# Kernel optimization log

Measured on AMD Instinct MI355X. Metric: run time of the kernel, lower is better.

Reference implementation:

```python
import jax, jax.numpy as jnp
import numpy as np
import math


def setup_inputs() -> dict:
    key = jax.random.key(0)
    ks = jax.random.split(key, 10)
    B, N, C, heads = 16, 1024, 256, 8
    nW = 4
    ANGLE_BINS = 5
    inner = C  # dim_head*heads == dim
    return {
        "x": jax.random.normal(ks[0], (B, N, C), jnp.float32),
        "mask": jax.random.normal(ks[1], (nW, N, N), jnp.float32),
        "affine_matrix": jax.random.normal(ks[2], (B, 2, 3), jnp.float32),
        "Wq": jax.random.normal(ks[3], (C, inner), jnp.float32) * (C ** -0.5),
        "bq": jnp.zeros((inner,), jnp.float32),
        "Wkv": jax.random.normal(ks[4], (C, 2 * inner), jnp.float32) * (C ** -0.5),
        "bkv": jnp.zeros((2 * inner,), jnp.float32),
        "Wp": jax.random.normal(ks[5], (C, C), jnp.float32) * (C ** -0.5),
        "bp": jnp.zeros((C,), jnp.float32),
        "angle_table": jnp.ones((ANGLE_BINS, heads), jnp.float32),
        "H": 32,
        "W": 32,
    }


def reference(x, mask, affine_matrix, Wq, bq, Wkv, bkv, Wp, bp, angle_table, H, W):
    B, N, C = x.shape
    heads = angle_table.shape[1]
    hd = C // heads
    scale = hd ** -0.5

    # qkv projections (torch Linear -> x @ W + b with W stored as (in, out))
    q = (x @ Wq + bq).reshape(B, N, heads, hd).transpose(0, 2, 1, 3)      # (B,h,N,d)
    kv = (x @ Wkv + bkv).reshape(B, N, 2, heads, hd).transpose(2, 0, 3, 1, 4)
    k, v = kv[0], kv[1]                                                    # (B,h,N,d)

    attn = jnp.einsum('bhqd,bhkd->bhqk', q * scale, k)                     # (B,h,N,N)

    # angle bias: per-query multiplicative bias in (1,2)
    grid_y, grid_x = jnp.meshgrid(jnp.arange(H), jnp.arange(W), indexing='ij')
    coords = jnp.stack([grid_x.reshape(-1), grid_y.reshape(-1)], -1).astype(jnp.float32)  # (N,2)
    center = jnp.array([W / 2.0, H / 2.0], jnp.float32)
    ego = jnp.einsum('bij,j->bi', affine_matrix[:, :2, :2], center) + affine_matrix[:, :2, 2]  # (B,2)
    rel = coords[None, :, :] - ego[:, None, :]                             # (B,N,2)
    ang = jnp.arctan2(rel[..., 1], rel[..., 0])
    bins = (((ang + math.pi) / (2.0 * math.pi)) * (angle_table.shape[0] - 1)).astype(jnp.int32)
    bias = 1.0 + jax.nn.sigmoid(angle_table[bins])                         # (B,N,h)
    attn = attn * bias.transpose(0, 2, 1)[..., None]                       # broadcast over keys

    # additive window mask then softmax
    nW = mask.shape[0]
    attn = attn.reshape(B // nW, nW, heads, N, N) + mask[None, :, None]
    attn = jax.nn.softmax(attn.reshape(B, heads, N, N), axis=-1)

    out = jnp.einsum('bhqk,bhkd->bhqd', attn, v).transpose(0, 2, 1, 3).reshape(B, N, C)
    return out @ Wp + bp
```

## Files before the change

kernel.cpp:

```cpp
#include <hip/hip_runtime.h>
#include <hip/hip_bf16.h>
#include <math.h>

#define BB 16
#define NTOK 1024
#define CDIM 256
#define HEADS 8
#define HD 32
#define LOG2E 1.4426950408889634f
#define PSHIFT 18.0f

typedef __attribute__((ext_vector_type(8))) _Float16 half8;
typedef __attribute__((ext_vector_type(8))) unsigned short u16x8;
typedef __attribute__((ext_vector_type(4))) unsigned int u32x4;
typedef __attribute__((ext_vector_type(4))) float f32x4;

__device__ __forceinline__ unsigned short f2h(float f) {
  _Float16 h = (_Float16)f;
  return __builtin_bit_cast(unsigned short, h);
}
__device__ __forceinline__ half8 ldh8(const unsigned short* p) {
  return *reinterpret_cast<const half8*>(p);
}
__device__ __forceinline__ void gl_lds16(const void* g, void* l) {
  __builtin_amdgcn_global_load_lds(
      (const __attribute__((address_space(1))) unsigned int*)g,
      (__attribute__((address_space(3))) unsigned int*)l, 16, 0, 0);
}

__global__ __launch_bounds__(256) void prep_xwb(
    const float* __restrict__ X, const float* __restrict__ Wq,
    const float* __restrict__ Wkv, const float* __restrict__ Wp,
    const float* __restrict__ affine, const float* __restrict__ atab,
    unsigned short* __restrict__ x16, unsigned short* __restrict__ wt16,
    unsigned short* __restrict__ wp16, float* __restrict__ bias) {
  int bid = blockIdx.x;
  if (bid < 2048) {
    size_t base = ((size_t)bid * 256 + threadIdx.x) * 8;
    float4 a = *(const float4*)(X + base);
    float4 b = *(const float4*)(X + base + 4);
    u16x8 o = {f2h(a.x), f2h(a.y), f2h(a.z), f2h(a.w),
               f2h(b.x), f2h(b.y), f2h(b.z), f2h(b.w)};
    *(u16x8*)(x16 + base) = o;
  } else if (bid < 3072) {
    int idx = (bid - 2048) * 256 + threadIdx.x;
    float val; size_t dst; bool isp = false;
    if (idx < 65536) {
      int k = idx >> 8, n = idx & 255;
      val = Wq[idx]; dst = (size_t)n * 256 + k;
    } else if (idx < 196608) {
      int i2 = idx - 65536;
      int k = i2 >> 9, n2 = i2 & 511;
      val = Wkv[i2]; dst = (size_t)(256 + n2) * 256 + k;
    } else {
      int i3 = idx - 196608;
      int k = i3 >> 8, n = i3 & 255;
      val = Wp[i3]; dst = (size_t)n * 256 + k; isp = true;
    }
    unsigned short h = f2h(val);
    if (isp) wp16[dst] = h; else wt16[dst] = h;
  } else {
    int idx = (bid - 3072) * 256 + threadIdx.x;
    if (idx >= BB * NTOK) return;
    int b = idx >> 10, n = idx & (NTOK - 1);
    float cx = (float)(n & 31);
    float cy = (float)(n >> 5);
    const float* A = affine + b * 6;
    float egx = fmaf(A[0], 16.f, fmaf(A[1], 16.f, A[2]));
    float egy = fmaf(A[3], 16.f, fmaf(A[4], 16.f, A[5]));
    float ang = atan2f(cy - egy, cx - egx);
    float t = (ang + 3.14159265358979323846f) *
              (1.f / (2.f * 3.14159265358979323846f)) * 4.f;
    int bin = (int)t;
    bin = bin < 0 ? 0 : (bin > 4 ? 4 : bin);
    for (int h = 0; h < HEADS; ++h) {
      float a = atab[bin * HEADS + h];
      float s = 1.f / (1.f + __expf(-a));
      bias[((size_t)b * HEADS + h) * NTOK + n] = 1.f + s;
    }
  }
}

__global__ __launch_bounds__(512, 4) void gemm_qkv16(
    const unsigned short* __restrict__ x16, const unsigned short* __restrict__ wt16,
    const float* __restrict__ bq, const float* __restrict__ bkv,
    const float* __restrict__ bias, const float* __restrict__ mask,
    unsigned short* __restrict__ q16, unsigned short* __restrict__ k16,
    unsigned short* __restrict__ vt16, float* __restrict__ mF32) {
  __shared__ __align__(16) unsigned short SM[16384];
  int bid = blockIdx.x;
  if (bid >= 768) {
    int idx = (bid - 768) * 512 + threadIdx.x;
    int b4 = idx >> 18;
    int rem = idx & 262143;
    int q = rem >> 8;
    int k = (rem & 255) * 4;
    float4 v = *(const float4*)(mask + ((size_t)b4 * NTOK + q) * NTOK + k);
    int kt = k >> 5;
    size_t off = (size_t)q * 16 + ((k & 31) >> 1);
    size_t slabE = ((size_t)(b4 * 64 + kt * 2)) * 16384;
    float2 e = {fmaf(v.x, LOG2E, -PSHIFT), fmaf(v.z, LOG2E, -PSHIFT)};
    float2 o = {fmaf(v.y, LOG2E, -PSHIFT), fmaf(v.w, LOG2E, -PSHIFT)};
    *(float2*)(mF32 + slabE + off) = e;
    *(float2*)(mF32 + slabE + 16384 + off) = o;
    return;
  }
  unsigned short* Xs = SM;
  unsigned short* Ws = SM + 8192;
  int tid = threadIdx.x;
  int w = tid >> 6, l = tid & 63;
  int row16 = l & 15, grp = l >> 4;
  int xcd = bid & 7, local = bid >> 3;
  int jb = local % 6, mb = xcd * 16 + local / 6;
  int j0 = jb * 128, m0 = mb * 128;
  int wm = w >> 1, wn = w & 1;

  auto stg = [&](int nb, int kt) {
    int k0s = kt * 32;
    int row = w * 16 + (l >> 2);
    int ge = (((l & 3) * 16) ^ ((row & 3) << 4)) >> 1;
    gl_lds16(x16 + (size_t)(m0 + row) * 256 + k0s + ge, Xs + nb * 4096 + w * 512);
    gl_lds16(wt16 + (size_t)(j0 + row) * 256 + k0s + ge, Ws + nb * 4096 + w * 512);
  };
  auto off16 = [&](int row, int g) {
    return row * 32 + ((((g * 16) ^ ((row & 3) << 4))) >> 1);
  };

  stg(0, 0);
  __syncthreads();

  f32x4 acc[2][4];
#pragma unroll
  for (int i = 0; i < 2; ++i)
#pragma unroll
    for (int c = 0; c < 4; ++c) acc[i][c] = (f32x4){0.f, 0.f, 0.f, 0.f};

  for (int kt = 0; kt < 8; ++kt) {
    int cur = kt & 1;
    if (kt < 7) stg(cur ^ 1, kt + 1);
    half8 a0 = ldh8(Xs + cur * 4096 + off16(wm * 32 + row16, grp));
    half8 a1 = ldh8(Xs + cur * 4096 + off16(wm * 32 + 16 + row16, grp));
#pragma unroll
    for (int c = 0; c < 4; ++c) {
      half8 bh = ldh8(Ws + cur * 4096 + off16(wn * 64 + c * 16 + row16, grp));
      acc[0][c] = __builtin_amdgcn_mfma_f32_16x16x32_f16(a0, bh, acc[0][c], 0, 0, 0);
      acc[1][c] = __builtin_amdgcn_mfma_f32_16x16x32_f16(a1, bh, acc[1][c], 0, 0, 0);
    }
    __syncthreads();
  }

  const float scaleq = 0.17677669529663687f * LOG2E;
  int half_mine = wm >> 1;
  for (int half = 0; half < 2; ++half) {
    if (half_mine == half) {
#pragma unroll
      for (int i = 0; i < 2; ++i) {
#pragma unroll
        for (int c = 0; c < 4; ++c) {
          int col = wn * 64 + c * 16 + row16;
          int jg = j0 + col;
#pragma unroll
          for (int r = 0; r < 4; ++r) {
            int rowl = (wm & 1) * 32 + i * 16 + grp * 4 + r;
            int m = m0 + half * 64 + rowl;
            int b = m >> 10, n = m & (NTOK - 1);
            float val = acc[i][c][r];
            unsigned short o;
            if (jb < 2)
              o = f2h((val + bq[jg]) * scaleq *
                      bias[((size_t)b * HEADS + (jg >> 5)) * NTOK + n]);
            else
              o = f2h(val + bkv[jg - CDIM]);
            SM[rowl * 136 + col] = o;
          }
        }
      }
    }
    __syncthreads();
    if (jb < 4) {
#pragma unroll
      for (int it = 0; it < 2; ++it) {
        int lin = it * 512 + tid;
        int rowb = lin >> 4, oct = lin & 15;
        u16x8 v = *(const u16x8*)&SM[rowb * 136 + oct * 8];
        int m = m0 + half * 64 + rowb;
        int b = m >> 10, n = m & (NTOK - 1);
        int jg = j0 + oct * 8;
        unsigned short* dst; int h, d;
        if (jb < 2) { h = jg >> 5; d = jg & 31; dst = q16; }
        else { int c2 = jg - CDIM; h = c2 >> 5; d = c2 & 31; dst = k16; }
        *(u16x8*)(dst + (((size_t)b * HEADS + h) * NTOK + n) * HD + d) = v;
      }
    } else {
#pragma unroll
      for (int it = 0; it < 2; ++it) {
        int lin = it * 512 + tid;
        int noct = lin >> 7, jl = lin & 127;
        u16x8 v;
#pragma unroll
        for (int e = 0; e < 8; ++e) v[e] = SM[(noct * 8 + e) * 136 + jl];
        int c3 = j0 + jl - 2 * CDIM;
        int h = c3 >> 5, d = c3 & 31;
        int n0 = m0 + half * 64 + noct * 8;
        int b = n0 >> 10, nn = n0 & (NTOK - 1);
        *(u16x8*)(vt16 + (((size_t)b * HEADS + h) * HD + d) * NTOK + nn) = v;
      }
    }
    __syncthreads();
  }
}

__global__ __launch_bounds__(512, 8) void attn16(
    const unsigned short* __restrict__ q16, const unsigned short* __restrict__ k16,
    const unsigned short* __restrict__ vt16, const float* __restrict__ mF32,
    unsigned short* __restrict__ ao16) {
  __shared__ __align__(16) unsigned short KT[2][2][1024];
  __shared__ __align__(16) unsigned short VT[2][2][1024];
  __shared__ __align__(16) float MT[2][2][1024];

  int tid = threadIdx.x;
  int w = tid >> 6, l = tid & 63;
  int row16 = l & 15, grp = l >> 4;
  int bid = blockIdx.x;
  int g = (bid >> 7) * 8 + (bid & 7);
  int inner = (bid >> 3) & 15;
  int qt = g >> 2, b4 = g & 3;
  int brep = inner >> 2, hg = inner & 3;
  int b = brep * 4 + b4;
  int hl = w & 1, role = w >> 1;
  int head = hg * 2 + hl;
  int bh = b * HEADS + head;
  int q0g = qt * 64;

  half8 bq16 = ldh8(q16 + ((size_t)bh * NTOK + q0g + role * 16 + row16) * HD +
                    grp * 8);

  const float* mFb = mF32 + (size_t)b4 * 64 * 16384;

  f32x4 acc[2];
  acc[0] = (f32x4){0.f, 0.f, 0.f, 0.f};
  acc[1] = (f32x4){0.f, 0.f, 0.f, 0.f};
  f32x4 accL = (f32x4){0.f, 0.f, 0.f, 0.f};
  const _Float16 one = (_Float16)1.0f;
  const half8 vones = {one, one, one, one, one, one, one, one};

  auto off32 = [&](int row, int gg) {
    return row * 32 + ((gg ^ ((row >> 1) & 3)) << 3);
  };

  auto stage = [&](int nb, int kt2) {
    int k0n = (kt2 & 31) * 32;
    if (role < 2) {
      int c = role;
      int r = c * 16 + (l >> 2);
      int key = 2 * (l >> 2) + c;
      int sk = (l & 3) ^ ((r >> 1) & 3);
      gl_lds16(k16 + ((size_t)bh * NTOK + k0n + key) * HD + sk * 8,
               &KT[nb][hl][c * 512]);
    } else {
      int c = role - 2;
      int dl = c * 16 + (l >> 2);
      int sv = (l & 3) ^ ((dl >> 1) & 3);
      gl_lds16(vt16 + ((size_t)bh * HD + dl) * NTOK + k0n + sv * 8,
               &VT[nb][hl][c * 512]);
    }
    {
      int slab = w >> 2, ch = w & 3;
      gl_lds16(mFb + (size_t)((kt2 & 31) * 2 + slab) * 16384 + q0g * 16 +
                   ch * 256 + l * 4,
               &MT[nb][slab][ch * 256]);
    }
  };

  stage(0, 0);
  __syncthreads();

  for (int kt = 0; kt < 32; ++kt) {
    int cur = kt & 1;
    if (kt < 31) stage(cur ^ 1, kt + 1);

    half8 kf0 = ldh8(&KT[cur][hl][off32(row16, grp)]);
    half8 kf1 = ldh8(&KT[cur][hl][off32(16 + row16, grp)]);
    half8 v0 = ldh8(&VT[cur][hl][off32(row16, grp)]);
    half8 v1 = ldh8(&VT[cur][hl][off32(16 + row16, grp)]);

    int qr = role * 16 + row16;
    f32x4 mC0 = *(const f32x4*)&MT[cur][0][qr * 16 + grp * 4];
    f32x4 mC1 = *(const f32x4*)&MT[cur][1][qr * 16 + grp * 4];
    f32x4 s0 = __builtin_amdgcn_mfma_f32_16x16x32_f16(kf0, bq16, mC0, 0, 0, 0);
    f32x4 s1 = __builtin_amdgcn_mfma_f32_16x16x32_f16(kf1, bq16, mC1, 0, 0, 0);
    f32x4 e0, e1;
#pragma unroll
    for (int r = 0; r < 4; ++r) {
      e0[r] = __builtin_amdgcn_exp2f(s0[r]);
      e1[r] = __builtin_amdgcn_exp2f(s1[r]);
    }
    u32x4 pk;
#pragma unroll
    for (int r = 0; r < 4; ++r)
      pk[r] = __builtin_bit_cast(unsigned,
                                 __builtin_amdgcn_cvt_pkrtz(e0[r], e1[r]));
    half8 pa = __builtin_bit_cast(half8, pk);
    acc[0] = __builtin_amdgcn_mfma_f32_16x16x32_f16(pa, v0, acc[0], 0, 0, 0);
    acc[1] = __builtin_amdgcn_mfma_f32_16x16x32_f16(pa, v1, acc[1], 0, 0, 0);
    accL = __builtin_amdgcn_mfma_f32_16x16x32_f16(pa, vones, accL, 0, 0, 0);
    __syncthreads();
  }

#pragma unroll
  for (int r = 0; r < 4; ++r) {
    float inv = 1.f / accL[r];
    int qrow = q0g + role * 16 + grp * 4 + r;
    size_t obase = ((size_t)b * NTOK + qrow) * CDIM + head * HD;
    ao16[obase + row16] = f2h(acc[0][r] * inv);
    ao16[obase + 16 + row16] = f2h(acc[1][r] * inv);
  }
}

__global__ __launch_bounds__(512, 4) void gemm_out16(
    const unsigned short* __restrict__ a16, const unsigned short* __restrict__ wp16,
    const float* __restrict__ bp, float* __restrict__ out) {
  __shared__ __align__(16) unsigned short SM[16384];
  unsigned short* Xs = SM;
  unsigned short* Ws = SM + 8192;
  int tid = threadIdx.x;
  int w = tid >> 6, l = tid & 63;
  int row16 = l & 15, grp = l >> 4;
  int bid = blockIdx.x;
  int xcd = bid & 7, local = bid >> 3;
  int jb = local & 1, mb = xcd * 16 + (local >> 1);
  int j0 = jb * 128, m0 = mb * 128;
  int wm = w >> 1, wn = w & 1;

  auto stg = [&](int nb, int kt) {
    int k0s = kt * 32;
    int row = w * 16 + (l >> 2);
    int ge = (((l & 3) * 16) ^ ((row & 3) << 4)) >> 1;
    gl_lds16(a16 + (size_t)(m0 + row) * 256 + k0s + ge, Xs + nb * 4096 + w * 512);
    gl_lds16(wp16 + (size_t)(j0 + row) * 256 + k0s + ge, Ws + nb * 4096 + w * 512);
  };
  auto off16 = [&](int row, int g) {
    return row * 32 + ((((g * 16) ^ ((row & 3) << 4))) >> 1);
  };

  stg(0, 0);
  __syncthreads();

  f32x4 acc[2][4];
#pragma unroll
  for (int i = 0; i < 2; ++i)
#pragma unroll
    for (int c = 0; c < 4; ++c) acc[i][c] = (f32x4){0.f, 0.f, 0.f, 0.f};

  for (int kt = 0; kt < 8; ++kt) {
    int cur = kt & 1;
    if (kt < 7) stg(cur ^ 1, kt + 1);
    half8 a0 = ldh8(Xs + cur * 4096 + off16(wm * 32 + row16, grp));
    half8 a1 = ldh8(Xs + cur * 4096 + off16(wm * 32 + 16 + row16, grp));
#pragma unroll
    for (int c = 0; c < 4; ++c) {
      half8 bh = ldh8(Ws + cur * 4096 + off16(wn * 64 + c * 16 + row16, grp));
      acc[0][c] = __builtin_amdgcn_mfma_f32_16x16x32_f16(a0, bh, acc[0][c], 0, 0, 0);
      acc[1][c] = __builtin_amdgcn_mfma_f32_16x16x32_f16(a1, bh, acc[1][c], 0, 0, 0);
    }
    __syncthreads();
  }

#pragma unroll
  for (int i = 0; i < 2; ++i) {
    int ng = m0 + wm * 32 + i * 16 + grp * 4;
#pragma unroll
    for (int c = 0; c < 4; ++c) {
      int jg = j0 + wn * 64 + c * 16 + row16;
      float bias = bp[jg];
#pragma unroll
      for (int r = 0; r < 4; ++r) {
        out[(size_t)(ng + r) * CDIM + jg] = acc[i][c][r] + bias;
      }
    }
  }
}

extern "C" void kernel_launch(void* const* d_in, const int* in_sizes, int n_in,
                              void* d_out, int out_size, void* d_ws,
                              size_t ws_size, hipStream_t stream) {
  const float* x = (const float*)d_in[0];
  const float* mask = (const float*)d_in[1];
  const float* affine = (const float*)d_in[2];
  const float* Wq = (const float*)d_in[3];
  const float* bq = (const float*)d_in[4];
  const float* Wkv = (const float*)d_in[5];
  const float* bkv = (const float*)d_in[6];
  const float* Wp = (const float*)d_in[7];
  const float* bp = (const float*)d_in[8];
  const float* atab = (const float*)d_in[9];
  float* out = (float*)d_out;

  const size_t bhnd = (size_t)BB * HEADS * NTOK * HD;
  unsigned short* q16 = (unsigned short*)d_ws;
  unsigned short* k16 = q16 + bhnd;
  unsigned short* vt16 = k16 + bhnd;
  unsigned short* x16 = vt16 + bhnd;
  unsigned short* wt16 = x16 + bhnd;
  unsigned short* wp16 = wt16 + 768 * 256;
  float* mF32 = (float*)(wp16 + 256 * 256);
  float* bias = mF32 + (size_t)4 * 64 * 16384;

  prep_xwb<<<3136, 256, 0, stream>>>(x, Wq, Wkv, Wp, affine, atab, x16, wt16,
                                     wp16, bias);
  gemm_qkv16<<<2816, 512, 0, stream>>>(x16, wt16, bq, bkv, bias, mask, q16,
                                       k16, vt16, mF32);
  attn16<<<1024, 512, 0, stream>>>(q16, k16, vt16, mF32, x16);
  gemm_out16<<<256, 512, 0, stream>>>(x16, wp16, bp, out);
}
```

Measured before the change: 82.50 us.

## Read raw mask directly in attention instead of pre-permuted copy

Removes the pre-pass that rewrote the 16 MB fp32 mask into a permuted, pre-scaled layout inside the QKV GEMM launch. The attention kernel now loads raw mask rows into LDS with an XOR swizzle, shuffles the values into the MFMA accumulator layout, and applies the log2e scale and shift to the scores before exp2. This saves one full write and read of the mask buffer. In exchange the inner loop gains an extra FMA per score, some register shuffling, and a changed scale on q, which alters numerics slightly.

```diff
diff --git a/kernel.cpp b/kernel.cpp
--- a/kernel.cpp
+++ b/kernel.cpp
@@ -84,27 +84,10 @@
 __global__ __launch_bounds__(512, 4) void gemm_qkv16(
     const unsigned short* __restrict__ x16, const unsigned short* __restrict__ wt16,
     const float* __restrict__ bq, const float* __restrict__ bkv,
-    const float* __restrict__ bias, const float* __restrict__ mask,
-    unsigned short* __restrict__ q16, unsigned short* __restrict__ k16,
-    unsigned short* __restrict__ vt16, float* __restrict__ mF32) {
+    const float* __restrict__ bias, unsigned short* __restrict__ q16,
+    unsigned short* __restrict__ k16, unsigned short* __restrict__ vt16) {
   __shared__ __align__(16) unsigned short SM[16384];
   int bid = blockIdx.x;
-  if (bid >= 768) {
-    int idx = (bid - 768) * 512 + threadIdx.x;
-    int b4 = idx >> 18;
-    int rem = idx & 262143;
-    int q = rem >> 8;
-    int k = (rem & 255) * 4;
-    float4 v = *(const float4*)(mask + ((size_t)b4 * NTOK + q) * NTOK + k);
-    int kt = k >> 5;
-    size_t off = (size_t)q * 16 + ((k & 31) >> 1);
-    size_t slabE = ((size_t)(b4 * 64 + kt * 2)) * 16384;
-    float2 e = {fmaf(v.x, LOG2E, -PSHIFT), fmaf(v.z, LOG2E, -PSHIFT)};
-    float2 o = {fmaf(v.y, LOG2E, -PSHIFT), fmaf(v.w, LOG2E, -PSHIFT)};
-    *(float2*)(mF32 + slabE + off) = e;
-    *(float2*)(mF32 + slabE + 16384 + off) = o;
-    return;
-  }
   unsigned short* Xs = SM;
   unsigned short* Ws = SM + 8192;
   int tid = threadIdx.x;
@@ -149,7 +132,7 @@
     __syncthreads();
   }
 
-  const float scaleq = 0.17677669529663687f * LOG2E;
+  const float scaleq = 0.17677669529663687f;
   int half_mine = wm >> 1;
   for (int half = 0; half < 2; ++half) {
     if (half_mine == half) {
@@ -212,11 +195,11 @@
 
 __global__ __launch_bounds__(512, 8) void attn16(
     const unsigned short* __restrict__ q16, const unsigned short* __restrict__ k16,
-    const unsigned short* __restrict__ vt16, const float* __restrict__ mF32,
+    const unsigned short* __restrict__ vt16, const float* __restrict__ mask,
     unsigned short* __restrict__ ao16) {
   __shared__ __align__(16) unsigned short KT[2][2][1024];
   __shared__ __align__(16) unsigned short VT[2][2][1024];
-  __shared__ __align__(16) float MT[2][2][1024];
+  __shared__ __align__(16) float MT[2][2048];
 
   int tid = threadIdx.x;
   int w = tid >> 6, l = tid & 63;
@@ -235,7 +218,7 @@
   half8 bq16 = ldh8(q16 + ((size_t)bh * NTOK + q0g + role * 16 + row16) * HD +
                     grp * 8);
 
-  const float* mFb = mF32 + (size_t)b4 * 64 * 16384;
+  const float* mbase = mask + (size_t)b4 * NTOK * NTOK;
 
   f32x4 acc[2];
   acc[0] = (f32x4){0.f, 0.f, 0.f, 0.f};
@@ -265,10 +248,10 @@
                &VT[nb][hl][c * 512]);
     }
     {
-      int slab = w >> 2, ch = w & 3;
-      gl_lds16(mFb + (size_t)((kt2 & 31) * 2 + slab) * 16384 + q0g * 16 +
-                   ch * 256 + l * 4,
-               &MT[nb][slab][ch * 256]);
+      int qq = w * 8 + (l >> 3);
+      int csrc = (l & 7) ^ (l >> 3);
+      gl_lds16(mbase + (size_t)(q0g + qq) * NTOK + k0n + csrc * 4,
+               &MT[nb][w * 256]);
     }
   };
 
@@ -285,15 +268,18 @@
     half8 v1 = ldh8(&VT[cur][hl][off32(16 + row16, grp)]);
 
     int qr = role * 16 + row16;
-    f32x4 mC0 = *(const f32x4*)&MT[cur][0][qr * 16 + grp * 4];
-    f32x4 mC1 = *(const f32x4*)&MT[cur][1][qr * 16 + grp * 4];
+    int q7 = qr & 7;
+    f32x4 mv0 = *(const f32x4*)&MT[cur][qr * 32 + (((2 * grp) ^ q7) << 2)];
+    f32x4 mv1 = *(const f32x4*)&MT[cur][qr * 32 + (((2 * grp + 1) ^ q7) << 2)];
+    f32x4 mC0 = (f32x4){mv0[0], mv0[2], mv1[0], mv1[2]};
+    f32x4 mC1 = (f32x4){mv0[1], mv0[3], mv1[1], mv1[3]};
     f32x4 s0 = __builtin_amdgcn_mfma_f32_16x16x32_f16(kf0, bq16, mC0, 0, 0, 0);
     f32x4 s1 = __builtin_amdgcn_mfma_f32_16x16x32_f16(kf1, bq16, mC1, 0, 0, 0);
     f32x4 e0, e1;
 #pragma unroll
     for (int r = 0; r < 4; ++r) {
-      e0[r] = __builtin_amdgcn_exp2f(s0[r]);
-      e1[r] = __builtin_amdgcn_exp2f(s1[r]);
+      e0[r] = __builtin_amdgcn_exp2f(fmaf(s0[r], LOG2E, -PSHIFT));
+      e1[r] = __builtin_amdgcn_exp2f(fmaf(s1[r], LOG2E, -PSHIFT));
     }
     u32x4 pk;
 #pragma unroll
@@ -403,13 +389,11 @@
   unsigned short* x16 = vt16 + bhnd;
   unsigned short* wt16 = x16 + bhnd;
   unsigned short* wp16 = wt16 + 768 * 256;
-  float* mF32 = (float*)(wp16 + 256 * 256);
-  float* bias = mF32 + (size_t)4 * 64 * 16384;
+  float* bias = (float*)(wp16 + 256 * 256);
 
   prep_xwb<<<3136, 256, 0, stream>>>(x, Wq, Wkv, Wp, affine, atab, x16, wt16,
                                      wp16, bias);
-  gemm_qkv16<<<2816, 512, 0, stream>>>(x16, wt16, bq, bkv, bias, mask, q16,
-                                       k16, vt16, mF32);
-  attn16<<<1024, 512, 0, stream>>>(q16, k16, vt16, mF32, x16);
+  gemm_qkv16<<<768, 512, 0, stream>>>(x16, wt16, bq, bkv, bias, q16, k16, vt16);
+  attn16<<<1024, 512, 0, stream>>>(q16, k16, vt16, mask, x16);
   gemm_out16<<<256, 512, 0, stream>>>(x16, wp16, bp, out);
 }
```

After: 86.41 us. 4.7% more time.
